# Performance work log

Measured on AMD Instinct MI355X. Metric: run time of the kernel, lower is better.

## Reference

```python
import jax, jax.numpy as jnp
import numpy as np

B, N, K, M, CIN, O, OUT = 4, 1024, 30, 8, 9, 64, 512
BN_SCALE = 1.0 / np.sqrt(1.0 + 1e-5)  # eval-mode BatchNorm with default stats/affine


def setup_inputs() -> dict:
    key = jax.random.key(0)
    ks = jax.random.split(key, 8)
    x = jax.random.normal(ks[0], (B, CIN, N), jnp.float32)
    norm_plt = jax.random.normal(ks[1], (B, 3, N), jnp.float32)
    cls_label = jnp.zeros((B, 16), jnp.float32)
    conv1_w = jax.random.normal(ks[2], (64, 18), jnp.float32) * np.sqrt(2.0 / 18.0)
    conv1_b = jnp.zeros((64,), jnp.float32)
    sn_hw = jax.random.normal(ks[3], (4, 16, 28), jnp.float32) * np.sqrt(2.0 / 28.0)
    sn_ow = jax.random.normal(ks[4], (4, M, 16), jnp.float32) * np.sqrt(2.0 / 16.0)
    sn_ob = jnp.zeros((4, M), jnp.float32)
    mats = jax.random.normal(ks[5], (4, 2 * O, M * O), jnp.float32) * np.sqrt(2.0 / (2.0 * O))
    convt_w = jax.random.normal(ks[6], (OUT, 5 * O), jnp.float32) * np.sqrt(2.0 / (5.0 * O))
    return dict(x=x, norm_plt=norm_plt, cls_label=cls_label, conv1_w=conv1_w,
                conv1_b=conv1_b, sn_hw=sn_hw, sn_ow=sn_ow, sn_ob=sn_ob,
                mats=mats, convt_w=convt_w)


def _gather(feat, idx):
    # feat (B,N,C), idx (B,N,K) int -> (B,N,K,C): neighbor feature gather
    return jax.vmap(lambda f, i: f[i])(feat, idx)


def _bn(t):
    return t * BN_SCALE


def reference(x, norm_plt, cls_label, conv1_w, conv1_b, sn_hw, sn_ow, sn_ob, mats, convt_w):
    xt = jnp.transpose(x, (0, 2, 1))                       # (B,N,9)
    sq = jnp.sum(xt * xt, axis=-1)
    neg_d = 2.0 * jnp.einsum('bic,bjc->bij', xt, xt) - sq[:, :, None] - sq[:, None, :]
    _, idx = jax.lax.top_k(neg_d, K)                       # (B,N,K) knn indices

    nbr = _gather(xt, idx)                                 # (B,N,K,9)
    ctr = jnp.broadcast_to(xt[:, :, None, :], nbr.shape)   # (B,N,K,9)
    diff = nbr - ctr
    ed = jnp.linalg.norm(diff, axis=-1, keepdims=True)     # (B,N,K,1)
    xyz = jnp.concatenate([diff, nbr, ctr, ed], axis=-1)   # (B,N,K,28) scorenet input

    # get_graph_feature -> conv1 (1x1) -> BN -> relu -> max over k
    gf = jnp.concatenate([diff, ctr], axis=-1)             # (B,N,K,18)
    h = jax.nn.relu(_bn(jnp.einsum('bnkc,oc->bnko', gf, conv1_w) + conv1_b))
    x1 = jnp.max(h, axis=2)                                # (B,N,64)

    feats = [x1]
    f = x1
    for l in range(4):  # PAConv layers 2..5 (sequential, fixed count)
        hid = jax.nn.relu(_bn(jnp.einsum('bnkc,hc->bnkh', xyz, sn_hw[l])))
        score = jax.nn.softmax(jnp.einsum('bnkh,mh->bnkm', hid, sn_ow[l]) + sn_ob[l], axis=-1)
        kern = mats[l]                                     # (128, M*64)
        # feat_trans_dgcnn: neighbor uses full kernel on [f;f], center uses top half
        point = (jnp.concatenate([f, f], axis=-1) @ kern).reshape(B, N, M, O)
        center = (f @ kern[:O]).reshape(B, N, M, O)
        # assemble_dgcnn: sum_k sum_m score * (point[knn] - center)
        gp = _gather(point.reshape(B, N, M * O), idx).reshape(B, N, K, M, O)
        out = jnp.einsum('bnkm,bnkmo->bno', score, gp) - jnp.einsum('bnkm,bnmo->bno', score, center)
        f = jax.nn.relu(_bn(out))
        feats.append(f)

    xx = jnp.concatenate(feats, axis=-1)                   # (B,N,320)
    xc = jax.nn.relu(_bn(jnp.einsum('bnc,oc->bno', xx, convt_w)))
    return jnp.max(xc, axis=1)                             # (B,512) global max pool
```

## Files before the change

kernel.cpp:

```cpp
#include <hip/hip_runtime.h>
#include <hip/hip_bf16.h>

#define B 4
#define N 1024
#define KNN 30
#define MM 8
#define OUTC 512
#define HID 16
#define FD 320
#define BNS 0.9999950000374997f

typedef float f32x4 __attribute__((ext_vector_type(4)));
typedef short s16x8 __attribute__((ext_vector_type(8)));

#define OFF_XT     0
#define OFF_SQ     36864
#define OFF_IDX    40960
#define OFF_CVT    163840
#define OFF_K2T    245760
#define OFF_FB     376832
#define OFF_SC     1032192

__global__ void __launch_bounds__(256) k_prep(const float* __restrict__ x,
                                              const float* __restrict__ convt_w,
                                              const float* __restrict__ mats,
                                              float* __restrict__ xt,
                                              float* __restrict__ sq,
                                              __hip_bfloat16* __restrict__ cvt_bf,
                                              __hip_bfloat16* __restrict__ k2t_bf,
                                              float* __restrict__ out) {
  __shared__ float tile[64][65];
  if (blockIdx.x < 640) {
    int id = blockIdx.x * 256 + threadIdx.x;
    if (id < B * N) {
      int b = id >> 10, n = id & 1023;
      float s = 0.f;
#pragma unroll
      for (int c = 0; c < 9; c++) {
        float v = x[(b * 9 + c) * N + n];
        xt[id * 9 + c] = v;
        s = fmaf(v, v, s);
      }
      sq[id] = s;
    }
    if (id < B * OUTC) out[id] = 0.f;
    if (id < 512 * 320) cvt_bf[id] = __float2bfloat16(convt_w[id]);
  } else {
    int blk = blockIdx.x - 640;
    int l = blk >> 4, part = (blk >> 3) & 1, m = blk & 7;
    int tr = threadIdx.x >> 6;
    int tc = threadIdx.x & 63;
    const float* src = mats + l * 65536 + (part * 64) * 512 + m * 64;
#pragma unroll
    for (int it = 0; it < 16; it++) {
      int c = it * 4 + tr;
      tile[c][tc] = src[c * 512 + tc];
    }
    __syncthreads();
    __hip_bfloat16* dst = k2t_bf + l * 65536 + part * 512 + m * 64;
#pragma unroll
    for (int it = 0; it < 16; it++) {
      int o = it * 4 + tr;
      dst[o * 1024 + tc] = __float2bfloat16(tile[tc][o]);
    }
  }
}

__global__ void __launch_bounds__(256) k_knnc1(const float* __restrict__ xt,
                                               const float* __restrict__ sq,
                                               const float* __restrict__ w,
                                               const float* __restrict__ bias,
                                               int* __restrict__ idx,
                                               __hip_bfloat16* __restrict__ feats_bf) {
  int t = threadIdx.x;
  int r = t >> 6;
  int lane = t & 63;
  int row = blockIdx.x * 4 + r;
  int b = row >> 10;
  __shared__ unsigned int hist[4][256];
  __shared__ unsigned int cntr[4];
  __shared__ unsigned int bp[4];
  __shared__ int bn[4];
  __shared__ int js_l[4][KNN];
  __shared__ float ws[64 * 18];
  __shared__ __align__(16) float diff_s[4][KNN][12];
  __shared__ float ctr_s[4][9];
  for (int i = t; i < 64 * 18; i += 256) ws[i] = w[i];
  if (t < 36) { int rr = t / 9, c = t - rr * 9; ctr_s[rr][c] = xt[(blockIdx.x * 4 + rr) * 9 + c]; }
  const float* xb = xt + (b << 10) * 9;
  const float* sb = sq + (b << 10);
  float cx[9];
#pragma unroll
  for (int c = 0; c < 9; c++) cx[c] = xt[row * 9 + c];
  float sqn = sq[row];
  unsigned int key[16];
#pragma unroll
  for (int s = 0; s < 16; s++) {
    int j = s * 64 + lane;
    const float* xj = xb + j * 9;
    float dot = 0.f;
#pragma unroll
    for (int c = 0; c < 9; c++) dot = fmaf(cx[c], xj[c], dot);
    float v = 2.0f * dot - sqn - sb[j];
    unsigned int u = __float_as_uint(v);
    key[s] = u ^ ((unsigned int)(((int)u) >> 31) | 0x80000000u);
  }
  if (lane == 0) cntr[r] = 0;
  unsigned int prefix = 0;
  int need = KNN;
  for (int p = 0; p < 4; p++) {
    int shift = 24 - 8 * p;
    for (int i = lane; i < 256; i += 64) hist[r][i] = 0;
    __syncthreads();
    unsigned int himask = (p == 0) ? 0u : (0xFFFFFFFFu << (shift + 8));
#pragma unroll
    for (int s = 0; s < 16; s++) {
      if ((key[s] & himask) == prefix)
        atomicAdd(&hist[r][(key[s] >> shift) & 255], 1u);
    }
    __syncthreads();
    int c0 = hist[r][4 * lane + 0], c1 = hist[r][4 * lane + 1];
    int c2 = hist[r][4 * lane + 2], c3 = hist[r][4 * lane + 3];
    int lsum = c0 + c1 + c2 + c3;
    int sfx = lsum;
#pragma unroll
    for (int ofs = 1; ofs < 64; ofs <<= 1) {
      int tt = __shfl_down(sfx, ofs, 64);
      if (lane + ofs < 64) sfx += tt;
    }
    int A3 = sfx - lsum;
    int A2 = A3 + c3, A1 = A2 + c2, A0 = A1 + c1;
    if (A0 < need && need <= A0 + c0) { bp[r] = prefix | ((unsigned)(4 * lane + 0) << shift); bn[r] = need - A0; }
    if (A1 < need && need <= A1 + c1) { bp[r] = prefix | ((unsigned)(4 * lane + 1) << shift); bn[r] = need - A1; }
    if (A2 < need && need <= A2 + c2) { bp[r] = prefix | ((unsigned)(4 * lane + 2) << shift); bn[r] = need - A2; }
    if (A3 < need && need <= A3 + c3) { bp[r] = prefix | ((unsigned)(4 * lane + 3) << shift); bn[r] = need - A3; }
    __syncthreads();
    prefix = bp[r];
    need = bn[r];
  }
  unsigned int T = prefix;
  int above_total = KNN - need;
  int* orow = idx + row * KNN;
#pragma unroll
  for (int s = 0; s < 16; s++) {
    if (key[s] > T) {
      unsigned int pslot = atomicAdd(&cntr[r], 1u);
      orow[pslot] = s * 64 + lane;
      js_l[r][pslot] = s * 64 + lane;
    }
  }
  int base = 0;
  for (int s = 0; s < 16; s++) {
    unsigned long long m = __ballot(key[s] == T);
    if (key[s] == T) {
      int rk = base + __popcll(m & ((1ull << lane) - 1ull));
      if (rk < need) {
        orow[above_total + rk] = s * 64 + lane;
        js_l[r][above_total + rk] = s * 64 + lane;
      }
    }
    base += __popcll(m);
    if (base >= need) break;
  }
  __syncthreads();
  if (t < 120) {
    int rr = t / KNN, k = t - rr * KNN;
    int j = js_l[rr][k];
    const float* xj = xt + ((b << 10) + j) * 9;
#pragma unroll
    for (int c = 0; c < 9; c++) diff_s[rr][k][c] = xj[c] - ctr_s[rr][c];
  }
  __syncthreads();
  float wd[9];
#pragma unroll
  for (int c = 0; c < 9; c++) wd[c] = ws[lane * 18 + c];
  float cd = 0.f;
#pragma unroll
  for (int c = 0; c < 9; c++) cd = fmaf(ctr_s[r][c], ws[lane * 18 + 9 + c], cd);
  float best = -3.0e38f;
  for (int k = 0; k < KNN; k++) {
    const float4* dr = (const float4*)diff_s[r][k];
    float4 d0 = dr[0], d1 = dr[1], d2v = dr[2];
    float dd = 0.f;
    dd = fmaf(d0.x, wd[0], dd); dd = fmaf(d0.y, wd[1], dd);
    dd = fmaf(d0.z, wd[2], dd); dd = fmaf(d0.w, wd[3], dd);
    dd = fmaf(d1.x, wd[4], dd); dd = fmaf(d1.y, wd[5], dd);
    dd = fmaf(d1.z, wd[6], dd); dd = fmaf(d1.w, wd[7], dd);
    dd = fmaf(d2v.x, wd[8], dd);
    best = fmaxf(best, dd);
  }
  float val = (best + cd + bias[lane]) * BNS;
  feats_bf[row * FD + lane] = __float2bfloat16(fmaxf(val, 0.f));
}

__global__ void __launch_bounds__(256) k_score(const float* __restrict__ xt,
                                               const int* __restrict__ idx,
                                               const float* __restrict__ hw,
                                               const float* __restrict__ ow,
                                               const float* __restrict__ ob,
                                               float* __restrict__ score) {
  __shared__ float hws[4 * 448];
  __shared__ float ows[4 * 128];
  __shared__ float obs[32];
  int t = threadIdx.x;
  for (int i = t; i < 1792; i += 256) hws[i] = hw[i];
  for (int i = t; i < 512; i += 256) ows[i] = ow[i];
  if (t < 32) obs[t] = ob[t];
  __syncthreads();
  int id = blockIdx.x * 256 + t;
  int row = id / KNN;
  int b = row >> 10;
  int j = idx[id];
  const float* xc = xt + row * 9;
  const float* xj = xt + ((b << 10) + j) * 9;
  float xv[28];
  float d2 = 0.f;
#pragma unroll
  for (int c = 0; c < 9; c++) {
    float nb = xj[c], ct = xc[c], df = nb - ct;
    xv[c] = df; xv[9 + c] = nb; xv[18 + c] = ct;
    d2 = fmaf(df, df, d2);
  }
  xv[27] = sqrtf(d2);
  for (int l = 0; l < 4; l++) {
    float hid[HID];
#pragma unroll
    for (int h = 0; h < HID; h++) {
      float a = 0.f;
#pragma unroll
      for (int c = 0; c < 28; c++) a = fmaf(xv[c], hws[l * 448 + h * 28 + c], a);
      hid[h] = fmaxf(a * BNS, 0.f);
    }
    float lg[MM], mx = -3.0e38f;
#pragma unroll
    for (int m = 0; m < MM; m++) {
      float a = obs[l * 8 + m];
#pragma unroll
      for (int h = 0; h < HID; h++) a = fmaf(hid[h], ows[l * 128 + m * 16 + h], a);
      lg[m] = a; mx = fmaxf(mx, a);
    }
    float s = 0.f;
#pragma unroll
    for (int m = 0; m < MM; m++) { lg[m] = __expf(lg[m] - mx); s += lg[m]; }
    float inv = 1.0f / s;
    float* so = score + l * 983040 + id * 8;
    *(float4*)so = make_float4(lg[0] * inv, lg[1] * inv, lg[2] * inv, lg[3] * inv);
    *(float4*)(so + 4) = make_float4(lg[4] * inv, lg[5] * inv, lg[6] * inv, lg[7] * inv);
  }
}

__global__ void __launch_bounds__(512) k_layer2(const int* __restrict__ idx,
                                                const float* __restrict__ score,
                                                const __hip_bfloat16* __restrict__ k2t_bf,
                                                __hip_bfloat16* __restrict__ feats_bf,
                                                const __hip_bfloat16* __restrict__ cvt_bf,
                                                float* __restrict__ out,
                                                int l, int last) {
  int row0 = blockIdx.x * 16;
  int t = threadIdx.x;
  int b = row0 >> 10;
  __shared__ int js[16][KNN];
  __shared__ float ssum[16][8];
  __shared__ __align__(16) __hip_bfloat16 Hs[16][1040];
  __shared__ __align__(16) __hip_bfloat16 ftile[16][336];
  const float* sc_l = score + l * 983040;
  for (int i = t; i < 16 * KNN; i += 512) {
    int r = i / KNN, k = i - r * KNN;
    js[r][k] = (b << 10) + idx[(row0 + r) * KNN + k];
  }
  if (t < 128) {
    int r = t >> 3, m = t & 7;
    float a = 0.f;
    for (int k = 0; k < KNN; k++) a += sc_l[(row0 + r) * 240 + k * 8 + m];
    ssum[r][m] = a;
  }
  __syncthreads();
  int wv = t >> 6, lane = t & 63;
#pragma unroll
  for (int rr = 0; rr < 2; rr++) {
    int r = wv * 2 + rr;
    int row = row0 + r;
    const float4* srow = (const float4*)(sc_l + row * 240);
    float g[MM] = {};
#pragma unroll
    for (int k = 0; k < KNN; k++) {
      float fv = __bfloat162float(feats_bf[js[r][k] * FD + l * 64 + lane]);
      float4 s0 = srow[2 * k], s1 = srow[2 * k + 1];
      g[0] = fmaf(s0.x, fv, g[0]); g[1] = fmaf(s0.y, fv, g[1]);
      g[2] = fmaf(s0.z, fv, g[2]); g[3] = fmaf(s0.w, fv, g[3]);
      g[4] = fmaf(s1.x, fv, g[4]); g[5] = fmaf(s1.y, fv, g[5]);
      g[6] = fmaf(s1.z, fv, g[6]); g[7] = fmaf(s1.w, fv, g[7]);
    }
    float fn = __bfloat162float(feats_bf[row * FD + l * 64 + lane]);
#pragma unroll
    for (int m = 0; m < MM; m++) {
      Hs[r][m * 64 + lane] = __float2bfloat16(g[m] - ssum[r][m] * fn);
      Hs[r][512 + m * 64 + lane] = __float2bfloat16(g[m]);
    }
  }
  __syncthreads();
  int lr = lane & 15, lk8 = (lane >> 4) * 8;
  if (wv < 4) {
    const short* Ks2 = (const short*)(k2t_bf + l * 65536);
    const short* brow = Ks2 + (wv * 16 + lr) * 1024 + lk8;
    const short* arow = (const short*)&Hs[lr][lk8];
    f32x4 acc = {0.f, 0.f, 0.f, 0.f};
#pragma unroll 8
    for (int kk = 0; kk < 32; kk++) {
      s16x8 a = *(const s16x8*)(arow + kk * 32);
      s16x8 bb = *(const s16x8*)(brow + kk * 32);
      acc = __builtin_amdgcn_mfma_f32_16x16x32_bf16(a, bb, acc, 0, 0, 0);
    }
    if (!last) {
#pragma unroll
      for (int i = 0; i < 4; i++) {
        int row = row0 + (lane >> 4) * 4 + i;
        feats_bf[row * FD + (l + 1) * 64 + wv * 16 + lr] =
            __float2bfloat16(fmaxf(acc[i] * BNS, 0.f));
      }
    } else {
#pragma unroll
      for (int i = 0; i < 4; i++) {
        int rl = (lane >> 4) * 4 + i;
        ftile[rl][256 + wv * 16 + lr] = __float2bfloat16(fmaxf(acc[i] * BNS, 0.f));
      }
    }
  } else if (last) {
    int t2 = t - 256;
    const short* Fs = (const short*)feats_bf;
    for (int i = t2; i < 512; i += 256) {
      int r = i >> 5, c8 = (i & 31) * 8;
      *(s16x8*)&ftile[r][c8] = *(const s16x8*)(Fs + (row0 + r) * FD + c8);
    }
  }
  if (last) {
    __syncthreads();
    const short* Ws = (const short*)cvt_bf;
#pragma unroll
    for (int tn = 0; tn < 4; tn++) {
      int nb = wv * 64 + tn * 16;
      const short* brow = Ws + (nb + lr) * FD + lk8;
      f32x4 acc = {0.f, 0.f, 0.f, 0.f};
#pragma unroll
      for (int kk = 0; kk < 10; kk++) {
        s16x8 a = *(const s16x8*)&ftile[lr][kk * 32 + lk8];
        s16x8 bb = *(const s16x8*)(brow + kk * 32);
        acc = __builtin_amdgcn_mfma_f32_16x16x32_bf16(a, bb, acc, 0, 0, 0);
      }
      float mx = fmaxf(fmaxf(acc[0], acc[1]), fmaxf(acc[2], acc[3]));
      mx = fmaxf(mx, __shfl_xor(mx, 16, 64));
      mx = fmaxf(mx, __shfl_xor(mx, 32, 64));
      if ((lane >> 4) == 0) {
        float val = fmaxf(mx * BNS, 0.f);
        atomicMax((unsigned int*)out + b * OUTC + nb + lr, __float_as_uint(val));
      }
    }
  }
}

extern "C" void kernel_launch(void* const* d_in, const int* in_sizes, int n_in,
                              void* d_out, int out_size, void* d_ws, size_t ws_size,
                              hipStream_t stream) {
  const float* x       = (const float*)d_in[0];
  const float* conv1_w = (const float*)d_in[3];
  const float* conv1_b = (const float*)d_in[4];
  const float* sn_hw   = (const float*)d_in[5];
  const float* sn_ow   = (const float*)d_in[6];
  const float* sn_ob   = (const float*)d_in[7];
  const float* mats    = (const float*)d_in[8];
  const float* convt_w = (const float*)d_in[9];
  float* out = (float*)d_out;

  float* w = (float*)d_ws;
  float* xt = w + OFF_XT;
  float* sq = w + OFF_SQ;
  int* idx = (int*)(w + OFF_IDX);
  __hip_bfloat16* cvt_bf = (__hip_bfloat16*)(w + OFF_CVT);
  __hip_bfloat16* k2t_bf = (__hip_bfloat16*)(w + OFF_K2T);
  __hip_bfloat16* feats_bf = (__hip_bfloat16*)(w + OFF_FB);
  float* score = w + OFF_SC;

  k_prep<<<704, 256, 0, stream>>>(x, convt_w, mats, xt, sq, cvt_bf, k2t_bf, out);
  k_knnc1<<<1024, 256, 0, stream>>>(xt, sq, conv1_w, conv1_b, idx, feats_bf);
  k_score<<<480, 256, 0, stream>>>(xt, idx, sn_hw, sn_ow, sn_ob, score);
  for (int l = 0; l < 4; l++) {
    k_layer2<<<256, 512, 0, stream>>>(idx, score, k2t_bf, feats_bf, cvt_bf, out,
                                      l, l == 3 ? 1 : 0);
  }
}
```

Before: 194.8 us.

## Fuse all stages into one cooperative persistent kernel with grid syncs

Replaces the seven separate launches (prep, knn+conv1, score, four layer kernels) with a single cooperative kernel of 256 blocks that uses grid.sync between dependent phases. Neighbor indices and softmax scores stay in LDS per block instead of going through global memory. The point data is also stored transposed and padded, and the layer GEMM is split across all 8 waves with a partial-sum reduction. The aim is to remove launch gaps and global round-trips. In exchange it needs a large LDS footprint with one block per CU and pays for grid-wide barriers.

```diff
diff --git a/kernel.cpp b/kernel.cpp
--- a/kernel.cpp
+++ b/kernel.cpp
@@ -1,349 +1,333 @@
 #include <hip/hip_runtime.h>
 #include <hip/hip_bf16.h>
+#include <hip/hip_cooperative_groups.h>
+
+namespace cg = cooperative_groups;
 
 #define B 4
 #define N 1024
 #define KNN 30
 #define MM 8
-#define OUTC 512
 #define HID 16
 #define FD 320
+#define OUTC 512
 #define BNS 0.9999950000374997f
 
 typedef float f32x4 __attribute__((ext_vector_type(4)));
 typedef short s16x8 __attribute__((ext_vector_type(8)));
 
-#define OFF_XT     0
-#define OFF_SQ     36864
-#define OFF_IDX    40960
-#define OFF_CVT    163840
-#define OFF_K2T    245760
-#define OFF_FB     376832
-#define OFF_SC     1032192
-
-__global__ void __launch_bounds__(256) k_prep(const float* __restrict__ x,
-                                              const float* __restrict__ convt_w,
-                                              const float* __restrict__ mats,
-                                              float* __restrict__ xt,
-                                              float* __restrict__ sq,
-                                              __hip_bfloat16* __restrict__ cvt_bf,
-                                              __hip_bfloat16* __restrict__ k2t_bf,
-                                              float* __restrict__ out) {
-  __shared__ float tile[64][65];
-  if (blockIdx.x < 640) {
-    int id = blockIdx.x * 256 + threadIdx.x;
-    if (id < B * N) {
-      int b = id >> 10, n = id & 1023;
-      float s = 0.f;
+#define OFF_XT16 0
+#define OFF_XTT  65536
+#define OFF_SQ   102400
+#define OFF_CVT  106496
+#define OFF_K2T  188416
+#define OFF_FB   319488
+
+#define L_JS    0
+#define L_SC    1920
+#define L_SSUM  63360
+#define L_FT    65408
+#define L_SCR   76160
+#define L_TILE  L_SCR
+#define L_HIST  L_SCR
+#define L_WS    L_SCR
+#define L_DIFF  (L_SCR+4608)
+#define L_HWS   L_SCR
+#define L_OWS   (L_SCR+7168)
+#define L_OBS   (L_SCR+9216)
+#define L_HS    L_SCR
+#define L_PACC  (L_SCR+33280)
+#define LDS_SZ  117632
+
+__global__ void __launch_bounds__(512, 1) k_fused(
+    const float* __restrict__ x, const float* __restrict__ convt_w,
+    const float* __restrict__ mats, const float* __restrict__ conv1_w,
+    const float* __restrict__ conv1_b, const float* __restrict__ hw,
+    const float* __restrict__ ow, const float* __restrict__ ob,
+    float* __restrict__ xt16, float* __restrict__ xtT, float* __restrict__ sq,
+    __hip_bfloat16* __restrict__ cvt_bf, __hip_bfloat16* __restrict__ k2t_bf,
+    __hip_bfloat16* __restrict__ feats_bf, float* __restrict__ out) {
+  cg::grid_group grid = cg::this_grid();
+  __shared__ __align__(16) char pool[LDS_SZ];
+  int* js = (int*)(pool + L_JS);
+  float* sc = (float*)(pool + L_SC);
+  float* ssum = (float*)(pool + L_SSUM);
+  __hip_bfloat16 (*ftile)[336] = (__hip_bfloat16(*)[336])(pool + L_FT);
+
+  int t = threadIdx.x;
+  int bid = blockIdx.x;
+  int row0 = bid * 16;
+  int b = row0 >> 10;
+  int w = t >> 6, lane = t & 63;
+
+  int gid = bid * 512 + t;
+  if (gid < B * N) {
+    int bb = gid >> 10, n = gid & 1023;
+    float s = 0.f;
+#pragma unroll
+    for (int c = 0; c < 9; c++) {
+      float v = x[(bb * 9 + c) * N + n];
+      xt16[gid * 16 + c] = v;
+      xtT[c * 4096 + gid] = v;
+      s = fmaf(v, v, s);
+    }
+    sq[gid] = s;
+  }
+  if (gid < B * OUTC) out[gid] = 0.f;
+  for (int i = gid; i < 512 * 320; i += 131072)
+    cvt_bf[i] = __float2bfloat16(convt_w[i]);
+  if (bid < 64) {
+    float (*tile)[65] = (float(*)[65])(pool + L_TILE);
+    int l = bid >> 4, part = (bid >> 3) & 1, m = bid & 7;
+    int tr = t >> 6, tc = t & 63;
+    const float* src = mats + l * 65536 + (part * 64) * 512 + m * 64;
+#pragma unroll
+    for (int it = 0; it < 8; it++) { int c = it * 8 + tr; tile[c][tc] = src[c * 512 + tc]; }
+    __syncthreads();
+    __hip_bfloat16* dst = k2t_bf + l * 65536 + part * 512 + m * 64;
+#pragma unroll
+    for (int it = 0; it < 8; it++) { int o = it * 8 + tr; dst[o * 1024 + tc] = __float2bfloat16(tile[tc][o]); }
+  }
+  grid.sync();
+
+  unsigned int* histw = (unsigned int*)(pool + L_HIST) + w * 256;
+  unsigned long long lowmask = (1ull << lane) - 1ull;
+  for (int rr = 0; rr < 2; rr++) {
+    int rloc = w * 2 + rr;
+    int row = row0 + rloc;
+    float cx[9];
+#pragma unroll
+    for (int c = 0; c < 9; c++) cx[c] = xt16[row * 16 + c];
+    float sqn = sq[row];
+    unsigned key[16];
+#pragma unroll
+    for (int s = 0; s < 16; s++) {
+      int j = s * 64 + lane;
+      float dot = 0.f;
+#pragma unroll
+      for (int c = 0; c < 9; c++) dot = fmaf(cx[c], xtT[c * 4096 + (b << 10) + j], dot);
+      float v = 2.0f * dot - sqn - sq[(b << 10) + j];
+      unsigned u = __float_as_uint(v);
+      key[s] = u ^ ((unsigned)(((int)u) >> 31) | 0x80000000u);
+    }
+    unsigned prefix = 0; int need = KNN;
+    for (int p = 0; p < 4; p++) {
+      int shift = 24 - 8 * p;
+#pragma unroll
+      for (int i = 0; i < 4; i++) histw[i * 64 + lane] = 0;
+      __syncthreads();
+      unsigned himask = p ? (0xFFFFFFFFu << (shift + 8)) : 0u;
+#pragma unroll
+      for (int s = 0; s < 16; s++)
+        if ((key[s] & himask) == prefix) atomicAdd(&histw[(key[s] >> shift) & 255], 1u);
+      __syncthreads();
+      int c0 = histw[4 * lane], c1 = histw[4 * lane + 1];
+      int c2 = histw[4 * lane + 2], c3 = histw[4 * lane + 3];
+      int lsum = c0 + c1 + c2 + c3, sfx = lsum;
+#pragma unroll
+      for (int ofs = 1; ofs < 64; ofs <<= 1) {
+        int tt2 = __shfl_down(sfx, ofs, 64);
+        if (lane + ofs < 64) sfx += tt2;
+      }
+      int A3 = sfx - lsum, A2 = A3 + c3, A1 = A2 + c2, A0 = A1 + c1;
+      unsigned candp = 0; int candn = 0; bool found = false;
+      if (A0 < need && need <= A0 + c0) { candp = prefix | ((unsigned)(4 * lane + 0) << shift); candn = need - A0; found = true; }
+      if (A1 < need && need <= A1 + c1) { candp = prefix | ((unsigned)(4 * lane + 1) << shift); candn = need - A1; found = true; }
+      if (A2 < need && need <= A2 + c2) { candp = prefix | ((unsigned)(4 * lane + 2) << shift); candn = need - A2; found = true; }
+      if (A3 < need && need <= A3 + c3) { candp = prefix | ((unsigned)(4 * lane + 3) << shift); candn = need - A3; found = true; }
+      unsigned long long fm = __ballot(found);
+      int srcl = __ffsll((unsigned long long)fm) - 1;
+      prefix = (unsigned)__shfl((int)candp, srcl, 64);
+      need = __shfl(candn, srcl, 64);
+    }
+    unsigned T = prefix;
+    int* jrow = js + rloc * KNN;
+    int aboveBase = 0;
+#pragma unroll
+    for (int s = 0; s < 16; s++) {
+      unsigned long long mA = __ballot(key[s] > T);
+      if (key[s] > T) jrow[aboveBase + __popcll(mA & lowmask)] = s * 64 + lane;
+      aboveBase += __popcll(mA);
+    }
+    int tieBase = 0;
+    for (int s = 0; s < 16 && tieBase < need; s++) {
+      unsigned long long mT = __ballot(key[s] == T);
+      if (key[s] == T) {
+        int rk = tieBase + __popcll(mT & lowmask);
+        if (rk < need) jrow[aboveBase + rk] = s * 64 + lane;
+      }
+      tieBase += __popcll(mT);
+    }
+  }
+  __syncthreads();
+
+  float* wsL = (float*)(pool + L_WS);
+  for (int i = t; i < 1152; i += 512) wsL[i] = conv1_w[i];
+  __syncthreads();
+  {
+    float wd[9], wc[9];
+#pragma unroll
+    for (int c = 0; c < 9; c++) { wd[c] = wsL[lane * 18 + c]; wc[c] = wsL[lane * 18 + 9 + c]; }
+    float bias = conv1_b[lane];
+    float* diffb = (float*)(pool + L_DIFF) + w * 360;
+    for (int rr = 0; rr < 2; rr++) {
+      int rloc = w * 2 + rr, row = row0 + rloc;
+      float ctr[9];
+#pragma unroll
+      for (int c = 0; c < 9; c++) ctr[c] = xt16[row * 16 + c];
+      if (lane < KNN) {
+        int jg = (b << 10) + js[rloc * KNN + lane];
+#pragma unroll
+        for (int c = 0; c < 9; c++) diffb[lane * 12 + c] = xt16[jg * 16 + c] - ctr[c];
+      }
+      __syncthreads();
+      float cd = 0.f;
+#pragma unroll
+      for (int c = 0; c < 9; c++) cd = fmaf(ctr[c], wc[c], cd);
+      float best = -3.0e38f;
+      for (int k = 0; k < KNN; k++) {
+        const f32x4* dr = (const f32x4*)&diffb[k * 12];
+        f32x4 d0 = dr[0], d1 = dr[1], d2 = dr[2];
+        float dd = 0.f;
+        dd = fmaf(d0.x, wd[0], dd); dd = fmaf(d0.y, wd[1], dd);
+        dd = fmaf(d0.z, wd[2], dd); dd = fmaf(d0.w, wd[3], dd);
+        dd = fmaf(d1.x, wd[4], dd); dd = fmaf(d1.y, wd[5], dd);
+        dd = fmaf(d1.z, wd[6], dd); dd = fmaf(d1.w, wd[7], dd);
+        dd = fmaf(d2.x, wd[8], dd);
+        best = fmaxf(best, dd);
+      }
+      float val = fmaxf((best + cd + bias) * BNS, 0.f);
+      __hip_bfloat16 vb = __float2bfloat16(val);
+      feats_bf[row * FD + lane] = vb;
+      ftile[rloc][lane] = vb;
+      __syncthreads();
+    }
+  }
+
+  {
+    float* hws = (float*)(pool + L_HWS);
+    float* ows = (float*)(pool + L_OWS);
+    float* obs = (float*)(pool + L_OBS);
+    for (int i = t; i < 1792; i += 512) hws[i] = hw[i];
+    if (t < 512) ows[t] = ow[t];
+    if (t < 32) obs[t] = ob[t];
+    __syncthreads();
+    if (t < 480) {
+      int r = t / KNN, k = t - r * KNN;
+      int row = row0 + r;
+      int jg = (b << 10) + js[r * KNN + k];
+      float xv[28]; float d2 = 0.f;
 #pragma unroll
       for (int c = 0; c < 9; c++) {
-        float v = x[(b * 9 + c) * N + n];
-        xt[id * 9 + c] = v;
-        s = fmaf(v, v, s);
-      }
-      sq[id] = s;
-    }
-    if (id < B * OUTC) out[id] = 0.f;
-    if (id < 512 * 320) cvt_bf[id] = __float2bfloat16(convt_w[id]);
-  } else {
-    int blk = blockIdx.x - 640;
-    int l = blk >> 4, part = (blk >> 3) & 1, m = blk & 7;
-    int tr = threadIdx.x >> 6;
-    int tc = threadIdx.x & 63;
-    const float* src = mats + l * 65536 + (part * 64) * 512 + m * 64;
-#pragma unroll
-    for (int it = 0; it < 16; it++) {
-      int c = it * 4 + tr;
-      tile[c][tc] = src[c * 512 + tc];
-    }
-    __syncthreads();
-    __hip_bfloat16* dst = k2t_bf + l * 65536 + part * 512 + m * 64;
-#pragma unroll
-    for (int it = 0; it < 16; it++) {
-      int o = it * 4 + tr;
-      dst[o * 1024 + tc] = __float2bfloat16(tile[tc][o]);
-    }
-  }
-}
-
-__global__ void __launch_bounds__(256) k_knnc1(const float* __restrict__ xt,
-                                               const float* __restrict__ sq,
-                                               const float* __restrict__ w,
-                                               const float* __restrict__ bias,
-                                               int* __restrict__ idx,
-                                               __hip_bfloat16* __restrict__ feats_bf) {
-  int t = threadIdx.x;
-  int r = t >> 6;
-  int lane = t & 63;
-  int row = blockIdx.x * 4 + r;
-  int b = row >> 10;
-  __shared__ unsigned int hist[4][256];
-  __shared__ unsigned int cntr[4];
-  __shared__ unsigned int bp[4];
-  __shared__ int bn[4];
-  __shared__ int js_l[4][KNN];
-  __shared__ float ws[64 * 18];
-  __shared__ __align__(16) float diff_s[4][KNN][12];
-  __shared__ float ctr_s[4][9];
-  for (int i = t; i < 64 * 18; i += 256) ws[i] = w[i];
-  if (t < 36) { int rr = t / 9, c = t - rr * 9; ctr_s[rr][c] = xt[(blockIdx.x * 4 + rr) * 9 + c]; }
-  const float* xb = xt + (b << 10) * 9;
-  const float* sb = sq + (b << 10);
-  float cx[9];
-#pragma unroll
-  for (int c = 0; c < 9; c++) cx[c] = xt[row * 9 + c];
-  float sqn = sq[row];
-  unsigned int key[16];
-#pragma unroll
-  for (int s = 0; s < 16; s++) {
-    int j = s * 64 + lane;
-    const float* xj = xb + j * 9;
-    float dot = 0.f;
-#pragma unroll
-    for (int c = 0; c < 9; c++) dot = fmaf(cx[c], xj[c], dot);
-    float v = 2.0f * dot - sqn - sb[j];
-    unsigned int u = __float_as_uint(v);
-    key[s] = u ^ ((unsigned int)(((int)u) >> 31) | 0x80000000u);
-  }
-  if (lane == 0) cntr[r] = 0;
-  unsigned int prefix = 0;
-  int need = KNN;
-  for (int p = 0; p < 4; p++) {
-    int shift = 24 - 8 * p;
-    for (int i = lane; i < 256; i += 64) hist[r][i] = 0;
-    __syncthreads();
-    unsigned int himask = (p == 0) ? 0u : (0xFFFFFFFFu << (shift + 8));
-#pragma unroll
-    for (int s = 0; s < 16; s++) {
-      if ((key[s] & himask) == prefix)
-        atomicAdd(&hist[r][(key[s] >> shift) & 255], 1u);
-    }
-    __syncthreads();
-    int c0 = hist[r][4 * lane + 0], c1 = hist[r][4 * lane + 1];
-    int c2 = hist[r][4 * lane + 2], c3 = hist[r][4 * lane + 3];
-    int lsum = c0 + c1 + c2 + c3;
-    int sfx = lsum;
-#pragma unroll
-    for (int ofs = 1; ofs < 64; ofs <<= 1) {
-      int tt = __shfl_down(sfx, ofs, 64);
-      if (lane + ofs < 64) sfx += tt;
-    }
-    int A3 = sfx - lsum;
-    int A2 = A3 + c3, A1 = A2 + c2, A0 = A1 + c1;
-    if (A0 < need && need <= A0 + c0) { bp[r] = prefix | ((unsigned)(4 * lane + 0) << shift); bn[r] = need - A0; }
-    if (A1 < need && need <= A1 + c1) { bp[r] = prefix | ((unsigned)(4 * lane + 1) << shift); bn[r] = need - A1; }
-    if (A2 < need && need <= A2 + c2) { bp[r] = prefix | ((unsigned)(4 * lane + 2) << shift); bn[r] = need - A2; }
-    if (A3 < need && need <= A3 + c3) { bp[r] = prefix | ((unsigned)(4 * lane + 3) << shift); bn[r] = need - A3; }
-    __syncthreads();
-    prefix = bp[r];
-    need = bn[r];
-  }
-  unsigned int T = prefix;
-  int above_total = KNN - need;
-  int* orow = idx + row * KNN;
-#pragma unroll
-  for (int s = 0; s < 16; s++) {
-    if (key[s] > T) {
-      unsigned int pslot = atomicAdd(&cntr[r], 1u);
-      orow[pslot] = s * 64 + lane;
-      js_l[r][pslot] = s * 64 + lane;
-    }
-  }
-  int base = 0;
-  for (int s = 0; s < 16; s++) {
-    unsigned long long m = __ballot(key[s] == T);
-    if (key[s] == T) {
-      int rk = base + __popcll(m & ((1ull << lane) - 1ull));
-      if (rk < need) {
-        orow[above_total + rk] = s * 64 + lane;
-        js_l[r][above_total + rk] = s * 64 + lane;
-      }
-    }
-    base += __popcll(m);
-    if (base >= need) break;
-  }
-  __syncthreads();
-  if (t < 120) {
-    int rr = t / KNN, k = t - rr * KNN;
-    int j = js_l[rr][k];
-    const float* xj = xt + ((b << 10) + j) * 9;
-#pragma unroll
-    for (int c = 0; c < 9; c++) diff_s[rr][k][c] = xj[c] - ctr_s[rr][c];
-  }
-  __syncthreads();
-  float wd[9];
-#pragma unroll
-  for (int c = 0; c < 9; c++) wd[c] = ws[lane * 18 + c];
-  float cd = 0.f;
-#pragma unroll
-  for (int c = 0; c < 9; c++) cd = fmaf(ctr_s[r][c], ws[lane * 18 + 9 + c], cd);
-  float best = -3.0e38f;
-  for (int k = 0; k < KNN; k++) {
-    const float4* dr = (const float4*)diff_s[r][k];
-    float4 d0 = dr[0], d1 = dr[1], d2v = dr[2];
-    float dd = 0.f;
-    dd = fmaf(d0.x, wd[0], dd); dd = fmaf(d0.y, wd[1], dd);
-    dd = fmaf(d0.z, wd[2], dd); dd = fmaf(d0.w, wd[3], dd);
-    dd = fmaf(d1.x, wd[4], dd); dd = fmaf(d1.y, wd[5], dd);
-    dd = fmaf(d1.z, wd[6], dd); dd = fmaf(d1.w, wd[7], dd);
-    dd = fmaf(d2v.x, wd[8], dd);
-    best = fmaxf(best, dd);
-  }
-  float val = (best + cd + bias[lane]) * BNS;
-  feats_bf[row * FD + lane] = __float2bfloat16(fmaxf(val, 0.f));
-}
-
-__global__ void __launch_bounds__(256) k_score(const float* __restrict__ xt,
-                                               const int* __restrict__ idx,
-                                               const float* __restrict__ hw,
-                                               const float* __restrict__ ow,
-                                               const float* __restrict__ ob,
-                                               float* __restrict__ score) {
-  __shared__ float hws[4 * 448];
-  __shared__ float ows[4 * 128];
-  __shared__ float obs[32];
-  int t = threadIdx.x;
-  for (int i = t; i < 1792; i += 256) hws[i] = hw[i];
-  for (int i = t; i < 512; i += 256) ows[i] = ow[i];
-  if (t < 32) obs[t] = ob[t];
-  __syncthreads();
-  int id = blockIdx.x * 256 + t;
-  int row = id / KNN;
-  int b = row >> 10;
-  int j = idx[id];
-  const float* xc = xt + row * 9;
-  const float* xj = xt + ((b << 10) + j) * 9;
-  float xv[28];
-  float d2 = 0.f;
-#pragma unroll
-  for (int c = 0; c < 9; c++) {
-    float nb = xj[c], ct = xc[c], df = nb - ct;
-    xv[c] = df; xv[9 + c] = nb; xv[18 + c] = ct;
-    d2 = fmaf(df, df, d2);
-  }
-  xv[27] = sqrtf(d2);
+        float nb = xt16[jg * 16 + c], ct = xt16[row * 16 + c], df = nb - ct;
+        xv[c] = df; xv[9 + c] = nb; xv[18 + c] = ct;
+        d2 = fmaf(df, df, d2);
+      }
+      xv[27] = sqrtf(d2);
+      for (int l = 0; l < 4; l++) {
+        float hid[HID];
+#pragma unroll
+        for (int h = 0; h < HID; h++) {
+          float a = 0.f;
+#pragma unroll
+          for (int c = 0; c < 28; c++) a = fmaf(xv[c], hws[l * 448 + h * 28 + c], a);
+          hid[h] = fmaxf(a * BNS, 0.f);
+        }
+        float lg[MM], mx = -3.0e38f;
+#pragma unroll
+        for (int m = 0; m < MM; m++) {
+          float a = obs[l * 8 + m];
+#pragma unroll
+          for (int h = 0; h < HID; h++) a = fmaf(hid[h], ows[l * 128 + m * 16 + h], a);
+          lg[m] = a; mx = fmaxf(mx, a);
+        }
+        float s = 0.f;
+#pragma unroll
+        for (int m = 0; m < MM; m++) { lg[m] = __expf(lg[m] - mx); s += lg[m]; }
+        float inv = 1.0f / s;
+        float* so = sc + ((l * 16 + r) * KNN + k) * 8;
+#pragma unroll
+        for (int m = 0; m < MM; m++) so[m] = lg[m] * inv;
+      }
+    }
+    __syncthreads();
+    { int l = t >> 7, r = (t >> 3) & 15, m = t & 7;
+      float a = 0.f;
+      for (int k = 0; k < KNN; k++) a += sc[((l * 16 + r) * KNN + k) * 8 + m];
+      ssum[(l * 16 + r) * 8 + m] = a; }
+  }
+  grid.sync();
+
+  __hip_bfloat16 (*Hs)[1040] = (__hip_bfloat16(*)[1040])(pool + L_HS);
+  float* pacc = (float*)(pool + L_PACC);
+  int lr = lane & 15, lk8 = (lane >> 4) * 8;
   for (int l = 0; l < 4; l++) {
-    float hid[HID];
-#pragma unroll
-    for (int h = 0; h < HID; h++) {
-      float a = 0.f;
-#pragma unroll
-      for (int c = 0; c < 28; c++) a = fmaf(xv[c], hws[l * 448 + h * 28 + c], a);
-      hid[h] = fmaxf(a * BNS, 0.f);
-    }
-    float lg[MM], mx = -3.0e38f;
-#pragma unroll
-    for (int m = 0; m < MM; m++) {
-      float a = obs[l * 8 + m];
-#pragma unroll
-      for (int h = 0; h < HID; h++) a = fmaf(hid[h], ows[l * 128 + m * 16 + h], a);
-      lg[m] = a; mx = fmaxf(mx, a);
-    }
-    float s = 0.f;
-#pragma unroll
-    for (int m = 0; m < MM; m++) { lg[m] = __expf(lg[m] - mx); s += lg[m]; }
-    float inv = 1.0f / s;
-    float* so = score + l * 983040 + id * 8;
-    *(float4*)so = make_float4(lg[0] * inv, lg[1] * inv, lg[2] * inv, lg[3] * inv);
-    *(float4*)(so + 4) = make_float4(lg[4] * inv, lg[5] * inv, lg[6] * inv, lg[7] * inv);
-  }
-}
-
-__global__ void __launch_bounds__(512) k_layer2(const int* __restrict__ idx,
-                                                const float* __restrict__ score,
-                                                const __hip_bfloat16* __restrict__ k2t_bf,
-                                                __hip_bfloat16* __restrict__ feats_bf,
-                                                const __hip_bfloat16* __restrict__ cvt_bf,
-                                                float* __restrict__ out,
-                                                int l, int last) {
-  int row0 = blockIdx.x * 16;
-  int t = threadIdx.x;
-  int b = row0 >> 10;
-  __shared__ int js[16][KNN];
-  __shared__ float ssum[16][8];
-  __shared__ __align__(16) __hip_bfloat16 Hs[16][1040];
-  __shared__ __align__(16) __hip_bfloat16 ftile[16][336];
-  const float* sc_l = score + l * 983040;
-  for (int i = t; i < 16 * KNN; i += 512) {
-    int r = i / KNN, k = i - r * KNN;
-    js[r][k] = (b << 10) + idx[(row0 + r) * KNN + k];
-  }
-  if (t < 128) {
-    int r = t >> 3, m = t & 7;
-    float a = 0.f;
-    for (int k = 0; k < KNN; k++) a += sc_l[(row0 + r) * 240 + k * 8 + m];
-    ssum[r][m] = a;
-  }
-  __syncthreads();
-  int wv = t >> 6, lane = t & 63;
-#pragma unroll
-  for (int rr = 0; rr < 2; rr++) {
-    int r = wv * 2 + rr;
-    int row = row0 + r;
-    const float4* srow = (const float4*)(sc_l + row * 240);
-    float g[MM] = {};
-#pragma unroll
-    for (int k = 0; k < KNN; k++) {
-      float fv = __bfloat162float(feats_bf[js[r][k] * FD + l * 64 + lane]);
-      float4 s0 = srow[2 * k], s1 = srow[2 * k + 1];
-      g[0] = fmaf(s0.x, fv, g[0]); g[1] = fmaf(s0.y, fv, g[1]);
-      g[2] = fmaf(s0.z, fv, g[2]); g[3] = fmaf(s0.w, fv, g[3]);
-      g[4] = fmaf(s1.x, fv, g[4]); g[5] = fmaf(s1.y, fv, g[5]);
-      g[6] = fmaf(s1.z, fv, g[6]); g[7] = fmaf(s1.w, fv, g[7]);
-    }
-    float fn = __bfloat162float(feats_bf[row * FD + l * 64 + lane]);
-#pragma unroll
-    for (int m = 0; m < MM; m++) {
-      Hs[r][m * 64 + lane] = __float2bfloat16(g[m] - ssum[r][m] * fn);
-      Hs[r][512 + m * 64 + lane] = __float2bfloat16(g[m]);
-    }
-  }
-  __syncthreads();
-  int lr = lane & 15, lk8 = (lane >> 4) * 8;
-  if (wv < 4) {
-    const short* Ks2 = (const short*)(k2t_bf + l * 65536);
-    const short* brow = Ks2 + (wv * 16 + lr) * 1024 + lk8;
-    const short* arow = (const short*)&Hs[lr][lk8];
-    f32x4 acc = {0.f, 0.f, 0.f, 0.f};
+    for (int rr = 0; rr < 2; rr++) {
+      int rloc = w * 2 + rr;
+      const float* scrow = sc + ((l * 16 + rloc) * KNN) * 8;
+      float g[MM] = {};
+      for (int k = 0; k < KNN; k++) {
+        int jg = (b << 10) + js[rloc * KNN + k];
+        float fv = __bfloat162float(feats_bf[jg * FD + l * 64 + lane]);
+        const f32x4* s4 = (const f32x4*)(scrow + k * 8);
+        f32x4 s0 = s4[0], s1 = s4[1];
+        g[0] = fmaf(s0.x, fv, g[0]); g[1] = fmaf(s0.y, fv, g[1]);
+        g[2] = fmaf(s0.z, fv, g[2]); g[3] = fmaf(s0.w, fv, g[3]);
+        g[4] = fmaf(s1.x, fv, g[4]); g[5] = fmaf(s1.y, fv, g[5]);
+        g[6] = fmaf(s1.z, fv, g[6]); g[7] = fmaf(s1.w, fv, g[7]);
+      }
+      float fn = __bfloat162float(ftile[rloc][l * 64 + lane]);
+      const float* su = ssum + (l * 16 + rloc) * 8;
+#pragma unroll
+      for (int m = 0; m < MM; m++) {
+        Hs[rloc][m * 64 + lane] = __float2bfloat16(g[m] - su[m] * fn);
+        Hs[rloc][512 + m * 64 + lane] = __float2bfloat16(g[m]);
+      }
+    }
+    __syncthreads();
+    {
+      int ct = w & 3, kh = w >> 2;
+      const short* Ks2 = (const short*)(k2t_bf + l * 65536);
+      const short* brow = Ks2 + (ct * 16 + lr) * 1024 + kh * 512 + lk8;
+      const short* arow = (const short*)&Hs[lr][kh * 512 + lk8];
+      f32x4 acc = {0.f, 0.f, 0.f, 0.f};
 #pragma unroll 8
-    for (int kk = 0; kk < 32; kk++) {
-      s16x8 a = *(const s16x8*)(arow + kk * 32);
-      s16x8 bb = *(const s16x8*)(brow + kk * 32);
-      acc = __builtin_amdgcn_mfma_f32_16x16x32_bf16(a, bb, acc, 0, 0, 0);
-    }
-    if (!last) {
+      for (int kk = 0; kk < 16; kk++) {
+        s16x8 a = *(const s16x8*)(arow + kk * 32);
+        s16x8 bb = *(const s16x8*)(brow + kk * 32);
+        acc = __builtin_amdgcn_mfma_f32_16x16x32_bf16(a, bb, acc, 0, 0, 0);
+      }
+#pragma unroll
+      for (int i = 0; i < 4; i++)
+        pacc[(w * 16 + (lane >> 4) * 4 + i) * 16 + lr] = acc[i];
+    }
+    __syncthreads();
+    if (w < 4) {
 #pragma unroll
       for (int i = 0; i < 4; i++) {
-        int row = row0 + (lane >> 4) * 4 + i;
-        feats_bf[row * FD + (l + 1) * 64 + wv * 16 + lr] =
-            __float2bfloat16(fmaxf(acc[i] * BNS, 0.f));
-      }
-    } else {
-#pragma unroll
-      for (int i = 0; i < 4; i++) {
-        int rl = (lane >> 4) * 4 + i;
-        ftile[rl][256 + wv * 16 + lr] = __float2bfloat16(fmaxf(acc[i] * BNS, 0.f));
-      }
-    }
-  } else if (last) {
-    int t2 = t - 256;
-    const short* Fs = (const short*)feats_bf;
-    for (int i = t2; i < 512; i += 256) {
-      int r = i >> 5, c8 = (i & 31) * 8;
-      *(s16x8*)&ftile[r][c8] = *(const s16x8*)(Fs + (row0 + r) * FD + c8);
-    }
-  }
-  if (last) {
-    __syncthreads();
+        int ri = (lane >> 4) * 4 + i;
+        float v0 = pacc[(w * 16 + ri) * 16 + lr];
+        float v1 = pacc[((w + 4) * 16 + ri) * 16 + lr];
+        float val = fmaxf((v0 + v1) * BNS, 0.f);
+        __hip_bfloat16 vb = __float2bfloat16(val);
+        feats_bf[(row0 + ri) * FD + (l + 1) * 64 + w * 16 + lr] = vb;
+        ftile[ri][(l + 1) * 64 + w * 16 + lr] = vb;
+      }
+    }
+    if (l < 3) grid.sync(); else __syncthreads();
+  }
+
+  {
     const short* Ws = (const short*)cvt_bf;
 #pragma unroll
     for (int tn = 0; tn < 4; tn++) {
-      int nb = wv * 64 + tn * 16;
+      int nb = w * 64 + tn * 16;
       const short* brow = Ws + (nb + lr) * FD + lk8;
+      const short* arow = (const short*)&ftile[lr][lk8];
       f32x4 acc = {0.f, 0.f, 0.f, 0.f};
 #pragma unroll
       for (int kk = 0; kk < 10; kk++) {
-        s16x8 a = *(const s16x8*)&ftile[lr][kk * 32 + lk8];
+        s16x8 a = *(const s16x8*)(arow + kk * 32);
         s16x8 bb = *(const s16x8*)(brow + kk * 32);
         acc = __builtin_amdgcn_mfma_f32_16x16x32_bf16(a, bb, acc, 0, 0, 0);
       }
@@ -371,20 +355,17 @@
   const float* convt_w = (const float*)d_in[9];
   float* out = (float*)d_out;
 
-  float* w = (float*)d_ws;
-  float* xt = w + OFF_XT;
-  float* sq = w + OFF_SQ;
-  int* idx = (int*)(w + OFF_IDX);
-  __hip_bfloat16* cvt_bf = (__hip_bfloat16*)(w + OFF_CVT);
-  __hip_bfloat16* k2t_bf = (__hip_bfloat16*)(w + OFF_K2T);
-  __hip_bfloat16* feats_bf = (__hip_bfloat16*)(w + OFF_FB);
-  float* score = w + OFF_SC;
-
-  k_prep<<<704, 256, 0, stream>>>(x, convt_w, mats, xt, sq, cvt_bf, k2t_bf, out);
-  k_knnc1<<<1024, 256, 0, stream>>>(xt, sq, conv1_w, conv1_b, idx, feats_bf);
-  k_score<<<480, 256, 0, stream>>>(xt, idx, sn_hw, sn_ow, sn_ob, score);
-  for (int l = 0; l < 4; l++) {
-    k_layer2<<<256, 512, 0, stream>>>(idx, score, k2t_bf, feats_bf, cvt_bf, out,
-                                      l, l == 3 ? 1 : 0);
-  }
+  float* wsp = (float*)d_ws;
+  float* xt16 = wsp + OFF_XT16;
+  float* xtT  = wsp + OFF_XTT;
+  float* sq   = wsp + OFF_SQ;
+  __hip_bfloat16* cvt_bf = (__hip_bfloat16*)(wsp + OFF_CVT);
+  __hip_bfloat16* k2t_bf = (__hip_bfloat16*)(wsp + OFF_K2T);
+  __hip_bfloat16* feats_bf = (__hip_bfloat16*)(wsp + OFF_FB);
+
+  void* args[] = {(void*)&x, (void*)&convt_w, (void*)&mats, (void*)&conv1_w,
+                  (void*)&conv1_b, (void*)&sn_hw, (void*)&sn_ow, (void*)&sn_ob,
+                  (void*)&xt16, (void*)&xtT, (void*)&sq, (void*)&cvt_bf,
+                  (void*)&k2t_bf, (void*)&feats_bf, (void*)&out};
+  hipLaunchCooperativeKernel((void*)k_fused, dim3(256), dim3(512), args, 0, stream);
 }
```

Result: slower. 327.2 us (+68.0%).
